# Kernel tuning notes

Hardware: AMD Instinct MI355X
Metric: run time of the kernel (lower is better)

Reference implementation:

```python
import jax, jax.numpy as jnp
import numpy as np

B, L, H = 16, 2048, 1024

def setup_inputs() -> dict:
    key = jax.random.key(0)
    ks = jax.random.split(key, 8)
    s = 1.0 / np.sqrt(H)
    return {
        "query": jax.random.normal(ks[0], (B, L, H), jnp.float32),
        "key_t": jax.random.normal(ks[1], (B, L, H), jnp.float32),
        "value": jax.random.normal(ks[2], (B, L, H), jnp.float32),
        # nn.Linear(H, H, bias=False) weights, stored torch-style [out, in]
        "Wq": jax.random.uniform(ks[3], (H, H), jnp.float32, -s, s),
        "Wk": jax.random.uniform(ks[4], (H, H), jnp.float32, -s, s),
        "bias": jax.random.uniform(ks[5], (H,), jnp.float32, -0.1, 0.1),
        # nn.Linear(H, 1): weight [1, H] -> stored as vector [H], plus scalar bias
        "w_score": jax.random.uniform(ks[6], (H,), jnp.float32, -s, s),
        "b_score": jax.random.uniform(ks[7], (1,), jnp.float32, -s, s),
    }

def reference(query, key_t, value, Wq, Wk, bias, w_score, b_score):
    # score = score_proj(tanh(key_proj(key) + query_proj(query) + bias)).squeeze(-1)
    h = jnp.tanh(jnp.einsum('blh,oh->blo', key_t, Wk)
                 + jnp.einsum('blh,oh->blo', query, Wq)
                 + bias)                                  # [B, L, H]
    score = jnp.einsum('blh,h->bl', h, w_score) + b_score  # [B, L]
    attn = jax.nn.softmax(score, axis=-1)                  # [B, L]
    # bmm(attn[:,None,:], value) -> [B,1,H]; sum over dim=1 (size 1) is identity
    context = jnp.einsum('bl,blh->bh', attn, value)[:, None, :]  # [B, 1, H]
    return context, attn
```

## Files before the change

### kernel.cpp

```cpp
#include <hip/hip_runtime.h>
#include <hip/hip_bf16.h>
#include <math.h>

#define B_SZ 16
#define L_SZ 2048
#define H_SZ 1024
#define M_TOT (B_SZ * L_SZ)
#define N_TOT H_SZ
#define KD (2 * H_SZ)
#define LC 16
#define LCHUNK (L_SZ / LC)

#define BM2 256
#define BN2 256
#define BK2 64
#define NT2 (KD / BK2)
#define NBN2 (N_TOT / BN2)
#define NBM2 (M_TOT / BM2)

typedef short short8 __attribute__((ext_vector_type(8)));
typedef float f32x4 __attribute__((ext_vector_type(4)));

#define WS_FAST_BYTES (6ull * 1024 * 1024 + 2ull * (size_t)M_TOT * KD)

#define GL16(gp, lp)                                                        \
    __builtin_amdgcn_global_load_lds(                                       \
        (const __attribute__((address_space(1))) unsigned int*)(gp),        \
        (__attribute__((address_space(3))) unsigned int*)(lp), 16, 0, 0)

#define BARRIER() __builtin_amdgcn_s_barrier()
#define LGKM0()  asm volatile("s_waitcnt lgkmcnt(0)" ::: "memory")
#define VMCNT4() asm volatile("s_waitcnt vmcnt(4)" ::: "memory")
#define VMCNT0() asm volatile("s_waitcnt vmcnt(0)" ::: "memory")

static __device__ __forceinline__ unsigned short f2bf(float f) {
    unsigned int u = __builtin_bit_cast(unsigned int, f);
    u += 0x7FFFu + ((u >> 16) & 1u);
    return (unsigned short)(u >> 16);
}

static __device__ __forceinline__ short8 pack8(float4 x, float4 y) {
    short8 r;
    r[0] = (short)f2bf(x.x); r[1] = (short)f2bf(x.y);
    r[2] = (short)f2bf(x.z); r[3] = (short)f2bf(x.w);
    r[4] = (short)f2bf(y.x); r[5] = (short)f2bf(y.y);
    r[6] = (short)f2bf(y.z); r[7] = (short)f2bf(y.w);
    return r;
}

static __device__ __forceinline__ float fast_tanh(float x) {
    float e = __expf(2.0f * x);
    return 1.0f - 2.0f * __builtin_amdgcn_rcpf(e + 1.0f);
}

__global__ __launch_bounds__(256) void concat_bf16(
    const float* __restrict__ key, const float* __restrict__ query,
    const float* __restrict__ Wk, const float* __restrict__ Wq,
    unsigned short* __restrict__ Xb, unsigned short* __restrict__ Wb)
{
    long long e0 = ((long long)blockIdx.x * 256 + threadIdx.x) * 8;
    int row = (int)(e0 >> 11);
    int kk  = (int)(e0 & 2047);
    const float* a; const float* b; unsigned short* dst;
    if (row < M_TOT) { a = key; b = query; dst = Xb + e0; }
    else { row -= M_TOT; a = Wk; b = Wq; dst = Wb + (((long long)row << 11) | kk); }
    const float* src = (kk < H_SZ) ? (a + (size_t)row * H_SZ + kk)
                                   : (b + (size_t)row * H_SZ + (kk - H_SZ));
    float4 x = ((const float4*)src)[0];
    float4 y = ((const float4*)src)[1];
    *(short8*)dst = pack8(x, y);
}

__global__ __launch_bounds__(512, 2) void score_gemm_8ph(
    const unsigned short* __restrict__ Xb,
    const unsigned short* __restrict__ Wb,
    const float* __restrict__ bias,
    const float* __restrict__ wscore,
    float* __restrict__ spart)
{
    extern __shared__ char smem[];
    char* Albase = smem;
    char* Blbase = smem + 65536;

    const int t    = threadIdx.x;
    const int lane = t & 63;
    const int wid  = t >> 6;
    const int wr   = wid >> 2;
    const int wc   = wid & 3;

    const int id  = blockIdx.x;
    const int xcd = id & 7;
    const int j   = id >> 3;
    const int bn  = j & 3;
    const int bm  = xcd * 16 + (j >> 2);
    const int r0  = bm * BM2;
    const int c0  = bn * BN2;

    const int srow = lane >> 2;
    const int scol = ((lane & 3) * 8) ^ ((lane >= 32) ? 16 : 0);
    const size_t gA0 = (size_t)(r0 + (wid)     * 16 + srow) * KD + scol;
    const size_t gA1 = (size_t)(r0 + (8 + wid) * 16 + srow) * KD + scol;
    const size_t gB0 = (size_t)(c0 + (wid)     * 16 + srow) * KD + scol;
    const size_t gB1 = (size_t)(c0 + (8 + wid) * 16 + srow) * KD + scol;

    const int fr  = lane & 15;
    const int fk8 = (lane >> 4) * 8;
    const int subbyte = (fr * 64 + fk8 * 2) ^ ((fr & 8) << 2);
    const char* aL = Albase + wr * 8192 + subbyte;
    const char* bL = Blbase + wc * 4096 + subbyte;

#define STAGE_A(buf, khalf, kt_) do {                                        \
    int kpos = (((kt_) & 31) * 64) + (khalf) * 32;                           \
    GL16(Xb + gA0 + kpos, Albase + (((buf)*2 + (khalf))*16 + wid)*1024);     \
    GL16(Xb + gA1 + kpos, Albase + (((buf)*2 + (khalf))*16 + 8 + wid)*1024); \
} while (0)
#define STAGE_B(buf, khalf, kt_) do {                                        \
    int kpos = (((kt_) & 31) * 64) + (khalf) * 32;                           \
    GL16(Wb + gB0 + kpos, Blbase + (((buf)*2 + (khalf))*16 + wid)*1024);     \
    GL16(Wb + gB1 + kpos, Blbase + (((buf)*2 + (khalf))*16 + 8 + wid)*1024); \
} while (0)

    short8 a_f[4], b_f0[4], b_f1[4];
    f32x4 acc[8][4] = {};

#define LDA4(buf, ks, mh) do { _Pragma("unroll")                             \
    for (int m = 0; m < 4; ++m)                                              \
        a_f[m] = *(const short8*)(aL +                                       \
            (((buf)*2 + (ks))*16 + (mh)*4 + m) * 1024); } while (0)
#define LDB4(dst, buf, ks) do { _Pragma("unroll")                            \
    for (int n = 0; n < 4; ++n)                                              \
        dst[n] = *(const short8*)(bL +                                       \
            (((buf)*2 + (ks))*16 + n) * 1024); } while (0)
#define MM16(bff, mh) do {                                                   \
    __builtin_amdgcn_s_setprio(1);                                           \
    _Pragma("unroll")                                                        \
    for (int m = 0; m < 4; ++m) { _Pragma("unroll")                          \
        for (int n = 0; n < 4; ++n)                                          \
            acc[(mh)*4 + m][n] = __builtin_amdgcn_mfma_f32_16x16x32_bf16(    \
                a_f[m], bff[n], acc[(mh)*4 + m][n], 0, 0, 0); }              \
    __builtin_amdgcn_s_setprio(0); } while (0)

#define TILE(buf, u) do {                                                    \
    LDA4(buf, 0, 0); LDB4(b_f0, buf, 0); STAGE_A(1-(buf), 1, (u)+1);         \
    BARRIER(); LGKM0(); MM16(b_f0, 0); BARRIER();                            \
    LDA4(buf, 0, 1); STAGE_B(1-(buf), 1, (u)+1);                             \
    BARRIER(); LGKM0(); MM16(b_f0, 1); BARRIER();                            \
    LDA4(buf, 1, 0); LDB4(b_f1, buf, 1); STAGE_A(buf, 0, (u)+2);             \
    BARRIER(); LGKM0(); MM16(b_f1, 0); BARRIER();                            \
    LDA4(buf, 1, 1); STAGE_B(buf, 0, (u)+2);                                 \
    BARRIER(); LGKM0(); MM16(b_f1, 1); VMCNT4(); BARRIER();                  \
} while (0)

    STAGE_A(0, 0, 0); STAGE_B(0, 0, 0);
    STAGE_A(0, 1, 0); STAGE_B(0, 1, 0);
    STAGE_A(1, 0, 1); STAGE_B(1, 0, 1);
    VMCNT4(); BARRIER();

    for (int it = 0; it < NT2; it += 2) {
        TILE(0, it);
        TILE(1, it + 1);
    }

    VMCNT0();
    __syncthreads();

    float* part = (float*)smem;
    const int fg = lane >> 4;
    float wsv[4], bsv[4];
    #pragma unroll
    for (int n = 0; n < 4; ++n) {
        int cg = c0 + wc * 64 + n * 16 + fr;
        wsv[n] = wscore[cg];
        bsv[n] = bias[cg];
    }
    #pragma unroll
    for (int mm = 0; mm < 8; ++mm) {
        #pragma unroll
        for (int r = 0; r < 4; ++r) {
            float s = 0.f;
            #pragma unroll
            for (int n = 0; n < 4; ++n)
                s += wsv[n] * fast_tanh(acc[mm][n][r] + bsv[n]);
            s += __shfl_xor(s, 1, 64);
            s += __shfl_xor(s, 2, 64);
            s += __shfl_xor(s, 4, 64);
            s += __shfl_xor(s, 8, 64);
            if (fr == 0)
                part[wc * 256 + wr * 128 + mm * 16 + fg * 4 + r] = s;
        }
    }
    __syncthreads();
    if (t < 256) {
        float v = part[t] + part[256 + t] + part[512 + t] + part[768 + t];
        spart[(size_t)(r0 + t) * 4 + bn] = v;
    }

#undef STAGE_A
#undef STAGE_B
#undef LDA4
#undef LDB4
#undef MM16
#undef TILE
}

__global__ __launch_bounds__(256) void softmax_k(
    const float* __restrict__ spart,
    float* __restrict__ attn)
{
    __shared__ float sc[L_SZ];
    __shared__ float red[8];
    const int b = blockIdx.x, t = threadIdx.x;
    const int lane = t & 63, wid = t >> 6;

    float lmax = -1e30f;
    #pragma unroll
    for (int i = 0; i < 8; ++i) {
        int l = t + i * 256;
        float4 u = *(const float4*)(spart + ((size_t)b * L_SZ + l) * 4);
        float s = (u.x + u.y) + (u.z + u.w);
        sc[l] = s;
        lmax = fmaxf(lmax, s);
    }
    #pragma unroll
    for (int off = 32; off; off >>= 1) lmax = fmaxf(lmax, __shfl_xor(lmax, off, 64));
    if (lane == 0) red[wid] = lmax;
    __syncthreads();
    float bmax = fmaxf(fmaxf(red[0], red[1]), fmaxf(red[2], red[3]));

    float lsum = 0.f;
    #pragma unroll
    for (int i = 0; i < 8; ++i) {
        int l = t + i * 256;
        float e = expf(sc[l] - bmax);
        sc[l] = e;
        lsum += e;
    }
    #pragma unroll
    for (int off = 32; off; off >>= 1) lsum += __shfl_xor(lsum, off, 64);
    if (lane == 0) red[4 + wid] = lsum;
    __syncthreads();
    float inv = 1.f / (((red[4] + red[5]) + (red[6] + red[7])));

    #pragma unroll
    for (int i = 0; i < 8; ++i) {
        int l = t + i * 256;
        attn[(size_t)b * L_SZ + l] = sc[l] * inv;
    }
}

__global__ __launch_bounds__(256) void ctx_part_k(
    const float* __restrict__ attn, const float* __restrict__ value,
    float* __restrict__ cpart)
{
    const int bid = blockIdx.x;
    const int b   = bid >> 6;
    const int rem = bid & 63;
    const int hc  = rem >> 4;
    const int lc  = rem & 15;
    const int h   = hc * 256 + threadIdx.x;

    const float* ap = attn + (size_t)b * L_SZ + lc * LCHUNK;
    const float* vp = value + ((size_t)b * L_SZ + lc * LCHUNK) * H_SZ + h;
    float acc = 0.f;
    #pragma unroll 4
    for (int l = 0; l < LCHUNK; ++l)
        acc += ap[l] * vp[(size_t)l * H_SZ];
    cpart[((size_t)(b * LC + lc)) * H_SZ + h] = acc;
}

__global__ __launch_bounds__(256) void ctx_reduce_k(
    const float* __restrict__ cpart, float* __restrict__ ctx)
{
    const int idx = blockIdx.x * 256 + threadIdx.x;
    const int b = idx >> 10, h = idx & 1023;
    float s = 0.f;
    #pragma unroll
    for (int lc = 0; lc < LC; ++lc)
        s += cpart[((size_t)(b * LC + lc)) * H_SZ + h];
    ctx[idx] = s;
}

extern "C" void kernel_launch(void* const* d_in, const int* in_sizes, int n_in,
                              void* d_out, int out_size, void* d_ws, size_t ws_size,
                              hipStream_t stream) {
    const float* query  = (const float*)d_in[0];
    const float* key_t  = (const float*)d_in[1];
    const float* value  = (const float*)d_in[2];
    const float* Wq     = (const float*)d_in[3];
    const float* Wk     = (const float*)d_in[4];
    const float* bias   = (const float*)d_in[5];
    const float* wscore = (const float*)d_in[6];

    float* out      = (float*)d_out;
    float* ctx_out  = out;
    float* attn_out = out + B_SZ * H_SZ;

    char* ws = (char*)d_ws;
    unsigned short* Wb = (unsigned short*)ws;
    float* spart = (float*)(ws + 4ull * 1024 * 1024);
    float* cpart = (float*)(ws + 5ull * 1024 * 1024);
    unsigned short* Xb = (unsigned short*)(ws + 6ull * 1024 * 1024);

    (void)hipFuncSetAttribute((const void*)score_gemm_8ph,
                              hipFuncAttributeMaxDynamicSharedMemorySize, 131072);

    int nblk = ((M_TOT + N_TOT) * KD / 8) / 256;
    concat_bf16<<<nblk, 256, 0, stream>>>(key_t, query, Wk, Wq, Xb, Wb);

    score_gemm_8ph<<<NBM2 * NBN2, 512, 131072, stream>>>(Xb, Wb, bias, wscore, spart);

    softmax_k<<<B_SZ, 256, 0, stream>>>(spart, attn_out);
    ctx_part_k<<<B_SZ * 4 * LC, 256, 0, stream>>>(attn_out, value, cpart);
    ctx_reduce_k<<<(B_SZ * H_SZ) / 256, 256, 0, stream>>>(cpart, ctx_out);
}
```

Before: 222.2 us.

## Double-buffer LDS-to-register fragments to overlap ds_reads with MFMA

Adds a second set of A and B register fragments so the next sub-tile's LDS reads are issued before the current MFMA block runs. The explicit lgkmcnt(0) waits are removed, and the global-load wait moves to vmcnt(6) at different points in the schedule. The aim is to hide LDS read latency behind matrix-core work, at the cost of more VGPRs. Dropping the explicit lgkm waits relies on the compiler inserting waits, and the reordered barriers and vmcnt points could expose races on the LDS buffers.

```diff
diff --git a/kernel.cpp b/kernel.cpp
--- a/kernel.cpp
+++ b/kernel.cpp
@@ -29,8 +29,8 @@
         (__attribute__((address_space(3))) unsigned int*)(lp), 16, 0, 0)
 
 #define BARRIER() __builtin_amdgcn_s_barrier()
-#define LGKM0()  asm volatile("s_waitcnt lgkmcnt(0)" ::: "memory")
 #define VMCNT4() asm volatile("s_waitcnt vmcnt(4)" ::: "memory")
+#define VMCNT6() asm volatile("s_waitcnt vmcnt(6)" ::: "memory")
 #define VMCNT0() asm volatile("s_waitcnt vmcnt(0)" ::: "memory")
 
 static __device__ __forceinline__ unsigned short f2bf(float f) {
@@ -120,41 +120,43 @@
     GL16(Wb + gB1 + kpos, Blbase + (((buf)*2 + (khalf))*16 + 8 + wid)*1024); \
 } while (0)
 
-    short8 a_f[4], b_f0[4], b_f1[4];
+    short8 aA[4], aB[4], b0[4], b1[4];
     f32x4 acc[8][4] = {};
 
-#define LDA4(buf, ks, mh) do { _Pragma("unroll")                             \
+#define LDA4_TO(dst, buf, ks, mh) do { _Pragma("unroll")                     \
     for (int m = 0; m < 4; ++m)                                              \
-        a_f[m] = *(const short8*)(aL +                                       \
+        dst[m] = *(const short8*)(aL +                                       \
             (((buf)*2 + (ks))*16 + (mh)*4 + m) * 1024); } while (0)
-#define LDB4(dst, buf, ks) do { _Pragma("unroll")                            \
+#define LDB4_TO(dst, buf, ks) do { _Pragma("unroll")                         \
     for (int n = 0; n < 4; ++n)                                              \
         dst[n] = *(const short8*)(bL +                                       \
             (((buf)*2 + (ks))*16 + n) * 1024); } while (0)
-#define MM16(bff, mh) do {                                                   \
+#define MM16(aset, bset, mh) do {                                            \
     __builtin_amdgcn_s_setprio(1);                                           \
     _Pragma("unroll")                                                        \
     for (int m = 0; m < 4; ++m) { _Pragma("unroll")                          \
         for (int n = 0; n < 4; ++n)                                          \
             acc[(mh)*4 + m][n] = __builtin_amdgcn_mfma_f32_16x16x32_bf16(    \
-                a_f[m], bff[n], acc[(mh)*4 + m][n], 0, 0, 0); }              \
+                aset[m], bset[n], acc[(mh)*4 + m][n], 0, 0, 0); }            \
     __builtin_amdgcn_s_setprio(0); } while (0)
 
 #define TILE(buf, u) do {                                                    \
-    LDA4(buf, 0, 0); LDB4(b_f0, buf, 0); STAGE_A(1-(buf), 1, (u)+1);         \
-    BARRIER(); LGKM0(); MM16(b_f0, 0); BARRIER();                            \
-    LDA4(buf, 0, 1); STAGE_B(1-(buf), 1, (u)+1);                             \
-    BARRIER(); LGKM0(); MM16(b_f0, 1); BARRIER();                            \
-    LDA4(buf, 1, 0); LDB4(b_f1, buf, 1); STAGE_A(buf, 0, (u)+2);             \
-    BARRIER(); LGKM0(); MM16(b_f1, 0); BARRIER();                            \
-    LDA4(buf, 1, 1); STAGE_B(buf, 0, (u)+2);                                 \
-    BARRIER(); LGKM0(); MM16(b_f1, 1); VMCNT4(); BARRIER();                  \
+    LDA4_TO(aB, buf, 0, 1); STAGE_A(1-(buf), 1, (u)+1);                      \
+    BARRIER(); MM16(aA, b0, 0); VMCNT6(); BARRIER();                         \
+    LDA4_TO(aA, buf, 1, 0); LDB4_TO(b1, buf, 1); STAGE_B(1-(buf), 1, (u)+1); \
+    BARRIER(); MM16(aB, b0, 1); BARRIER();                                   \
+    LDA4_TO(aB, buf, 1, 1); STAGE_A(buf, 0, (u)+2);                          \
+    BARRIER(); MM16(aA, b1, 0); VMCNT6(); BARRIER();                         \
+    LDA4_TO(aA, 1-(buf), 0, 0); LDB4_TO(b0, 1-(buf), 0); STAGE_B(buf, 0, (u)+2); \
+    BARRIER(); MM16(aB, b1, 1); BARRIER();                                   \
 } while (0)
 
     STAGE_A(0, 0, 0); STAGE_B(0, 0, 0);
     STAGE_A(0, 1, 0); STAGE_B(0, 1, 0);
     STAGE_A(1, 0, 1); STAGE_B(1, 0, 1);
-    VMCNT4(); BARRIER();
+    VMCNT4();
+    BARRIER();
+    LDA4_TO(aA, 0, 0, 0); LDB4_TO(b0, 0, 0);
 
     for (int it = 0; it < NT2; it += 2) {
         TILE(0, it);
@@ -197,8 +199,8 @@
 
 #undef STAGE_A
 #undef STAGE_B
-#undef LDA4
-#undef LDB4
+#undef LDA4_TO
+#undef LDB4_TO
 #undef MM16
 #undef TILE
 }
```

After: 226.0 us. Within noise of the previous version (+1.7%).

## Fuse fp32-to-bf16 activation conversion into GEMM A-operand loading

Applied to the files above, without the earlier changes.

Removes the separate concat/convert pass over key and query: the GEMM now loads fp32 activations straight into registers, converts them to bf16, and writes them to LDS. Only the weights are still converted ahead of time in a small kernel. This avoids writing and re-reading a 128 MB bf16 intermediate. In exchange, A is read as fp32 (twice the bytes) by each of the four column blocks, uses more registers, and goes through register-staged LDS writes instead of direct global-to-LDS loads, which changes the pipeline's wait counts.

```diff
diff --git a/kernel.cpp b/kernel.cpp
--- a/kernel.cpp
+++ b/kernel.cpp
@@ -21,8 +21,6 @@
 typedef short short8 __attribute__((ext_vector_type(8)));
 typedef float f32x4 __attribute__((ext_vector_type(4)));
 
-#define WS_FAST_BYTES (6ull * 1024 * 1024 + 2ull * (size_t)M_TOT * KD)
-
 #define GL16(gp, lp)                                                        \
     __builtin_amdgcn_global_load_lds(                                       \
         (const __attribute__((address_space(1))) unsigned int*)(gp),        \
@@ -31,6 +29,7 @@
 #define BARRIER() __builtin_amdgcn_s_barrier()
 #define LGKM0()  asm volatile("s_waitcnt lgkmcnt(0)" ::: "memory")
 #define VMCNT4() asm volatile("s_waitcnt vmcnt(4)" ::: "memory")
+#define VMCNT6() asm volatile("s_waitcnt vmcnt(6)" ::: "memory")
 #define VMCNT0() asm volatile("s_waitcnt vmcnt(0)" ::: "memory")
 
 static __device__ __forceinline__ unsigned short f2bf(float f) {
@@ -53,26 +52,24 @@
     return 1.0f - 2.0f * __builtin_amdgcn_rcpf(e + 1.0f);
 }
 
-__global__ __launch_bounds__(256) void concat_bf16(
-    const float* __restrict__ key, const float* __restrict__ query,
-    const float* __restrict__ Wk, const float* __restrict__ Wq,
-    unsigned short* __restrict__ Xb, unsigned short* __restrict__ Wb)
-{
-    long long e0 = ((long long)blockIdx.x * 256 + threadIdx.x) * 8;
-    int row = (int)(e0 >> 11);
-    int kk  = (int)(e0 & 2047);
-    const float* a; const float* b; unsigned short* dst;
-    if (row < M_TOT) { a = key; b = query; dst = Xb + e0; }
-    else { row -= M_TOT; a = Wk; b = Wq; dst = Wb + (((long long)row << 11) | kk); }
-    const float* src = (kk < H_SZ) ? (a + (size_t)row * H_SZ + kk)
-                                   : (b + (size_t)row * H_SZ + (kk - H_SZ));
+__global__ __launch_bounds__(256) void conv_w(
+    const float* __restrict__ Wq, const float* __restrict__ Wk,
+    unsigned short* __restrict__ Wb)
+{
+    int idx = blockIdx.x * 256 + threadIdx.x;
+    int e0 = idx * 8;
+    int o  = e0 >> 11;
+    int kk = e0 & 2047;
+    const float* src = (kk < H_SZ) ? (Wk + (size_t)o * H_SZ + kk)
+                                   : (Wq + (size_t)o * H_SZ + (kk - H_SZ));
     float4 x = ((const float4*)src)[0];
     float4 y = ((const float4*)src)[1];
-    *(short8*)dst = pack8(x, y);
+    *(short8*)(Wb + e0) = pack8(x, y);
 }
 
 __global__ __launch_bounds__(512, 2) void score_gemm_8ph(
-    const unsigned short* __restrict__ Xb,
+    const float* __restrict__ keyg,
+    const float* __restrict__ qryg,
     const unsigned short* __restrict__ Wb,
     const float* __restrict__ bias,
     const float* __restrict__ wscore,
@@ -98,8 +95,6 @@
 
     const int srow = lane >> 2;
     const int scol = ((lane & 3) * 8) ^ ((lane >= 32) ? 16 : 0);
-    const size_t gA0 = (size_t)(r0 + (wid)     * 16 + srow) * KD + scol;
-    const size_t gA1 = (size_t)(r0 + (8 + wid) * 16 + srow) * KD + scol;
     const size_t gB0 = (size_t)(c0 + (wid)     * 16 + srow) * KD + scol;
     const size_t gB1 = (size_t)(c0 + (8 + wid) * 16 + srow) * KD + scol;
 
@@ -109,10 +104,24 @@
     const char* aL = Albase + wr * 8192 + subbyte;
     const char* bL = Blbase + wc * 4096 + subbyte;
 
-#define STAGE_A(buf, khalf, kt_) do {                                        \
-    int kpos = (((kt_) & 31) * 64) + (khalf) * 32;                           \
-    GL16(Xb + gA0 + kpos, Albase + (((buf)*2 + (khalf))*16 + wid)*1024);     \
-    GL16(Xb + gA1 + kpos, Albase + (((buf)*2 + (khalf))*16 + 8 + wid)*1024); \
+    const int arow0 = r0 + wid * 16 + (lane >> 2);
+    const int arow1 = r0 + (8 + wid) * 16 + (lane >> 2);
+    const int acsub = (lane & 3) * 8;
+    const int awbyte = (lane * 16) ^ (lane & 32);
+
+#define ALOAD(rr, khalf, kt_) do {                                           \
+    int koff = (((kt_) & 31) * 64) + (khalf) * 32 + acsub;                   \
+    const float* base_ = (koff < H_SZ) ? (keyg + koff)                       \
+                                       : (qryg + (koff - H_SZ));             \
+    const float* p0_ = base_ + (size_t)arow0 * H_SZ;                         \
+    const float* p1_ = base_ + (size_t)arow1 * H_SZ;                         \
+    rr[0] = ((const float4*)p0_)[0]; rr[1] = ((const float4*)p0_)[1];        \
+    rr[2] = ((const float4*)p1_)[0]; rr[3] = ((const float4*)p1_)[1];        \
+} while (0)
+#define AWRITE(rr, buf, khalf) do {                                          \
+    char* d_ = Albase + (((buf)*2 + (khalf))*16 + wid)*1024 + awbyte;        \
+    *(short8*)d_            = pack8(rr[0], rr[1]);                           \
+    *(short8*)(d_ + 8*1024) = pack8(rr[2], rr[3]);                           \
 } while (0)
 #define STAGE_B(buf, khalf, kt_) do {                                        \
     int kpos = (((kt_) & 31) * 64) + (khalf) * 32;                           \
@@ -120,6 +129,7 @@
     GL16(Wb + gB1 + kpos, Blbase + (((buf)*2 + (khalf))*16 + 8 + wid)*1024); \
 } while (0)
 
+    float4 rA0[4], rA1[4];
     short8 a_f[4], b_f0[4], b_f1[4];
     f32x4 acc[8][4] = {};
 
@@ -141,20 +151,25 @@
     __builtin_amdgcn_s_setprio(0); } while (0)
 
 #define TILE(buf, u) do {                                                    \
-    LDA4(buf, 0, 0); LDB4(b_f0, buf, 0); STAGE_A(1-(buf), 1, (u)+1);         \
+    LDA4(buf, 0, 0); LDB4(b_f0, buf, 0);                                     \
+    AWRITE(rA1, 1-(buf), 1); ALOAD(rA0, 0, (u)+2);                           \
     BARRIER(); LGKM0(); MM16(b_f0, 0); BARRIER();                            \
     LDA4(buf, 0, 1); STAGE_B(1-(buf), 1, (u)+1);                             \
     BARRIER(); LGKM0(); MM16(b_f0, 1); BARRIER();                            \
-    LDA4(buf, 1, 0); LDB4(b_f1, buf, 1); STAGE_A(buf, 0, (u)+2);             \
+    LDA4(buf, 1, 0); LDB4(b_f1, buf, 1);                                     \
+    AWRITE(rA0, buf, 0); ALOAD(rA1, 1, (u)+2);                               \
     BARRIER(); LGKM0(); MM16(b_f1, 0); BARRIER();                            \
     LDA4(buf, 1, 1); STAGE_B(buf, 0, (u)+2);                                 \
-    BARRIER(); LGKM0(); MM16(b_f1, 1); VMCNT4(); BARRIER();                  \
+    BARRIER(); LGKM0(); MM16(b_f1, 1); VMCNT6(); BARRIER();                  \
 } while (0)
 
-    STAGE_A(0, 0, 0); STAGE_B(0, 0, 0);
-    STAGE_A(0, 1, 0); STAGE_B(0, 1, 0);
-    STAGE_A(1, 0, 1); STAGE_B(1, 0, 1);
-    VMCNT4(); BARRIER();
+    STAGE_B(0, 0, 0); STAGE_B(0, 1, 0); STAGE_B(1, 0, 1);
+    ALOAD(rA0, 0, 0); ALOAD(rA1, 1, 0);
+    AWRITE(rA0, 0, 0); AWRITE(rA1, 0, 1);
+    ALOAD(rA0, 0, 1);  AWRITE(rA0, 1, 0);
+    ALOAD(rA1, 1, 1);
+    VMCNT4();
+    BARRIER();
 
     for (int it = 0; it < NT2; it += 2) {
         TILE(0, it);
@@ -195,7 +210,8 @@
         spart[(size_t)(r0 + t) * 4 + bn] = v;
     }
 
-#undef STAGE_A
+#undef ALOAD
+#undef AWRITE
 #undef STAGE_B
 #undef LDA4
 #undef LDB4
@@ -299,15 +315,14 @@
     unsigned short* Wb = (unsigned short*)ws;
     float* spart = (float*)(ws + 4ull * 1024 * 1024);
     float* cpart = (float*)(ws + 5ull * 1024 * 1024);
-    unsigned short* Xb = (unsigned short*)(ws + 6ull * 1024 * 1024);
 
     (void)hipFuncSetAttribute((const void*)score_gemm_8ph,
                               hipFuncAttributeMaxDynamicSharedMemorySize, 131072);
 
-    int nblk = ((M_TOT + N_TOT) * KD / 8) / 256;
-    concat_bf16<<<nblk, 256, 0, stream>>>(key_t, query, Wk, Wq, Xb, Wb);
-
-    score_gemm_8ph<<<NBM2 * NBN2, 512, 131072, stream>>>(Xb, Wb, bias, wscore, spart);
+    conv_w<<<1024, 256, 0, stream>>>(Wq, Wk, Wb);
+
+    score_gemm_8ph<<<NBM2 * NBN2, 512, 131072, stream>>>(
+        key_t, query, Wb, bias, wscore, spart);
 
     softmax_k<<<B_SZ, 256, 0, stream>>>(spart, attn_out);
     ctx_part_k<<<B_SZ * 4 * LC, 256, 0, stream>>>(attn_out, value, cpart);
```

New measurement: 234.5 us. 1.06x slower.
